# Optimization experiments

Measured on AMD Instinct MI355X. Metric: run time of the kernel, lower is better.

The kernel has to match this reference:

```python
import jax, jax.numpy as jnp
import numpy as np

B, T, C = 4, 2048, 768
H, D = 12, 64          # num heads, head size
MLP = 3072
EPS = 1e-6
SCALE = C ** (-0.5)    # NOTE: source scales by n_embd**-0.5, not head_size**-0.5


def setup_inputs() -> dict:
    key = jax.random.key(0)
    ks = jax.random.split(key, 12)
    s = 0.02
    return {
        "x":     jax.random.normal(ks[0], (B, T, C), jnp.float32),
        "Wq":    jax.random.normal(ks[1], (H, C, D), jnp.float32) * s,
        "Wk":    jax.random.normal(ks[2], (H, C, D), jnp.float32) * s,
        "Wv":    jax.random.normal(ks[3], (H, C, D), jnp.float32) * s,
        "Wo":    jax.random.normal(ks[4], (H * D, C), jnp.float32) * s,
        "bo":    jnp.zeros((C,), jnp.float32),
        "ln1_g": jnp.ones((C,), jnp.float32),
        "ln1_b": jnp.zeros((C,), jnp.float32),
        "ln2_g": jnp.ones((C,), jnp.float32),
        "ln2_b": jnp.zeros((C,), jnp.float32),
        "W1":    jax.random.normal(ks[5], (C, MLP), jnp.float32) * s,
        "b1":    jnp.zeros((MLP,), jnp.float32),
        "W2":    jax.random.normal(ks[6], (MLP, C), jnp.float32) * s,
        "b2":    jnp.zeros((C,), jnp.float32),
    }


def _ln(x, g, b):
    mu = jnp.mean(x, axis=-1, keepdims=True)
    var = jnp.var(x, axis=-1, keepdims=True)
    return (x - mu) * jax.lax.rsqrt(var + EPS) * g + b


def reference(x, Wq, Wk, Wv, Wo, bo, ln1_g, ln1_b, ln2_g, ln2_b, W1, b1, W2, b2):
    xn = _ln(x, ln1_g, ln1_b)
    # batched per-head projections: [B,T,C] x [H,C,D] -> [B,H,T,D]
    q = jnp.einsum("btc,hcd->bhtd", xn, Wq)
    k = jnp.einsum("btc,hcd->bhtd", xn, Wk)
    v = jnp.einsum("btc,hcd->bhtd", xn, Wv)
    wei = jnp.einsum("bhtd,bhsd->bhts", q, k) * SCALE  # [B,H,T,T]
    wei = jax.nn.softmax(wei, axis=-1)
    attn = jnp.einsum("bhts,bhsd->bhtd", wei, v)
    # concat heads along feature dim (head order preserved)
    attn = attn.transpose(0, 2, 1, 3).reshape(B, T, H * D)
    sa = attn @ Wo + bo
    x2 = sa + x                      # residual 1 (dropout = identity in eval)
    y = _ln(x2, ln2_g, ln2_b)
    y = jax.nn.gelu(y @ W1 + b1, approximate=False) @ W2 + b2
    return x2 + y                    # residual 2
```

## Files before the change

### kernel.cpp

```cpp
#include <hip/hip_runtime.h>
#include <hip/hip_bf16.h>
#include <cstdint>
#include <cmath>

#define B_ 4
#define T_ 2048
#define C_ 768
#define H_ 12
#define D_ 64
#define MLP_ 3072
#define BT_ (B_*T_)

typedef __hip_bfloat16 hbf;
typedef __bf16 bf16_t;
typedef bf16_t bf16x8 __attribute__((ext_vector_type(8)));
typedef bf16_t bf16x4 __attribute__((ext_vector_type(4)));
typedef float f32x4 __attribute__((ext_vector_type(4)));

static __device__ __forceinline__ void load_lds16(const void* g, void* l) {
    __builtin_amdgcn_global_load_lds(
        (const __attribute__((address_space(1))) unsigned int*)g,
        (__attribute__((address_space(3))) unsigned int*)l, 16, 0, 0);
}

__global__ __launch_bounds__(256) void pack_all(
    const float* __restrict__ Wq, const float* __restrict__ Wk,
    const float* __restrict__ Wv, const float* __restrict__ Wo,
    const float* __restrict__ W1, const float* __restrict__ W2,
    hbf* __restrict__ WqkT, hbf* __restrict__ WoT,
    hbf* __restrict__ W1T, hbf* __restrict__ W2T)
{
    __shared__ float tl[64 * 65];
    const int blk = blockIdx.x;
    const float* src; hbf* dst; int R, S, r0, s0;
    if (blk < 432) {
        const int z = blk / 12, y = blk - z * 12;
        const int mtx = z / 12, head = z - mtx * 12;
        src = (mtx == 0 ? Wq : mtx == 1 ? Wk : Wv) + (size_t)head * 49152;
        dst = WqkT + (size_t)z * 49152;
        R = 768; S = 64; r0 = y * 64; s0 = 0;
    } else if (blk < 576) {
        const int l = blk - 432;
        src = Wo; dst = WoT; R = 768; S = 768;
        r0 = (l / 12) * 64; s0 = (l % 12) * 64;
    } else if (blk < 1152) {
        const int l = blk - 576;
        src = W1; dst = W1T; R = 768; S = 3072;
        r0 = (l / 48) * 64; s0 = (l % 48) * 64;
    } else {
        const int l = blk - 1152;
        src = W2; dst = W2T; R = 3072; S = 768;
        r0 = (l / 12) * 64; s0 = (l % 12) * 64;
    }
    const int c = threadIdx.x & 63, q = threadIdx.x >> 6;
#pragma unroll
    for (int j = 0; j < 16; ++j) {
        int r = q + j * 4;
        tl[r * 65 + c] = src[(size_t)(r0 + r) * S + s0 + c];
    }
    __syncthreads();
#pragma unroll
    for (int j = 0; j < 16; ++j) {
        int s = q + j * 4;
        dst[(size_t)(s0 + s) * R + r0 + c] = __float2bfloat16(tl[c * 65 + s]);
    }
}

template<typename TI>
__global__ __launch_bounds__(192) void ln_kernel(
    const TI* __restrict__ x, const float* __restrict__ g,
    const float* __restrict__ bb, hbf* __restrict__ out)
{
    __shared__ float red[6];
    const int row = blockIdx.x;
    const int t = threadIdx.x;
    float v[4];
    if constexpr (__is_same(TI, float)) {
        const float4 xv = *(const float4*)(x + (size_t)row * C_ + t * 4);
        v[0] = xv.x; v[1] = xv.y; v[2] = xv.z; v[3] = xv.w;
    } else {
        bf16x4 xv = *(const bf16x4*)((const bf16_t*)x + (size_t)row * C_ + t * 4);
#pragma unroll
        for (int k = 0; k < 4; ++k) v[k] = (float)xv[k];
    }
    float s = 0.0f, s2 = 0.0f;
#pragma unroll
    for (int k = 0; k < 4; ++k) { s += v[k]; s2 += v[k] * v[k]; }
#pragma unroll
    for (int m = 1; m < 64; m <<= 1) {
        s  += __shfl_xor(s,  m, 64);
        s2 += __shfl_xor(s2, m, 64);
    }
    if ((t & 63) == 0) { red[t >> 6] = s; red[3 + (t >> 6)] = s2; }
    __syncthreads();
    float S  = red[0] + red[1] + red[2];
    float S2 = red[3] + red[4] + red[5];
    float mu  = S * (1.0f / C_);
    float var = S2 * (1.0f / C_) - mu * mu;
    float inv = rsqrtf(var + 1e-6f);
    const float4 gv = *(const float4*)(g  + t * 4);
    const float4 bv = *(const float4*)(bb + t * 4);
    bf16x4 o4;
    o4[0] = (bf16_t)((v[0] - mu) * inv * gv.x + bv.x);
    o4[1] = (bf16_t)((v[1] - mu) * inv * gv.y + bv.y);
    o4[2] = (bf16_t)((v[2] - mu) * inv * gv.z + bv.z);
    o4[3] = (bf16_t)((v[3] - mu) * inv * gv.w + bv.w);
    *(bf16x4*)((bf16_t*)out + (size_t)row * C_ + t * 4) = o4;
}

template<int EPI, int TN>
__global__ __launch_bounds__(256, 4) void gemm_kernel(
    const hbf* __restrict__ A, const hbf* __restrict__ Bt,
    float* __restrict__ outF, hbf* __restrict__ outH,
    const float* __restrict__ bias, const float* __restrict__ residF,
    const hbf* __restrict__ residH,
    int M, int N, int K,
    hbf* __restrict__ qb, hbf* __restrict__ kb, hbf* __restrict__ vt,
    float scale, int gx)
{
    constexpr int AM = (TN == 128) ? 4 : 2;
    constexpr int NB_B = (TN == 128) ? 4 : 2;
    __shared__ hbf sA[128 * 64];
    __shared__ hbf sB[TN * 64];
    const int tid = threadIdx.x;
    const int lane = tid & 63;
    const int wid = tid >> 6;
    const int lr = lane & 15, hg = lane >> 4;
    const int bid = blockIdx.x, nwg = gridDim.x;
    const int wg = (bid & 7) * (nwg >> 3) + (bid >> 3);
    const int bx = wg % gx, by = wg / gx;
    const int row0 = by * 128;
    const int col0 = bx * TN;
    const int wrow = (TN == 128) ? (wid >> 1) * 64 : wid * 32;
    const int wcol = (TN == 128) ? (wid & 1) * 64 : 0;

    f32x4 acc[AM][4] = {};

    int offG[4];
    const int Kb = K * 2;
#pragma unroll
    for (int i = 0; i < 4; ++i) {
        int c = tid + i * 256;
        offG[i] = (c >> 3) * Kb + (((c & 7) ^ ((c >> 3) & 7)) << 4);
    }
    const char* gA = (const char*)(A + (size_t)row0 * K);
    const char* gB = (const char*)(Bt + (size_t)col0 * K);

    auto stage = [&](int kt) {
        const int kb2 = kt * 128;
#pragma unroll
        for (int i = 0; i < 4; ++i)
            load_lds16(gA + (size_t)(offG[i] + kb2), (char*)sA + i * 4096 + wid * 1024);
#pragma unroll
        for (int i = 0; i < NB_B; ++i)
            load_lds16(gB + (size_t)(offG[i] + kb2), (char*)sB + i * 4096 + wid * 1024);
    };

    const int NK = K >> 6;
    stage(0);
    for (int kt = 0; kt < NK; ++kt) {
        __syncthreads();
#pragma unroll
        for (int kf = 0; kf < 2; ++kf) {
            const int sl = ((kf * 4 + hg) ^ (lr & 7)) << 4;
            bf16x8 af[AM], bfr[4];
#pragma unroll
            for (int m = 0; m < AM; ++m)
                af[m] = *(const bf16x8*)((const char*)sA + (wrow + m * 16 + lr) * 128 + sl);
#pragma unroll
            for (int n = 0; n < 4; ++n)
                bfr[n] = *(const bf16x8*)((const char*)sB + (wcol + n * 16 + lr) * 128 + sl);
#pragma unroll
            for (int m = 0; m < AM; ++m)
#pragma unroll
                for (int n = 0; n < 4; ++n)
                    acc[m][n] = __builtin_amdgcn_mfma_f32_16x16x32_bf16(af[m], bfr[n], acc[m][n], 0, 0, 0);
        }
        __syncthreads();
        if (kt + 1 < NK) stage(kt + 1);
    }

#pragma unroll
    for (int m = 0; m < AM; ++m) {
#pragma unroll
        for (int n = 0; n < 4; ++n) {
            const int colc = col0 + wcol + n * 16 + lr;
            const int rowb = row0 + wrow + m * 16 + hg * 4;
            if constexpr (EPI == 3) {
                if (colc >= 2 * C_) {
                    bf16x4 w;
#pragma unroll
                    for (int j = 0; j < 4; ++j) w[j] = (bf16_t)acc[m][n][j];
                    *(bf16x4*)(vt + (size_t)(colc - 2 * C_) * BT_ + rowb) = w;
                    continue;
                }
            }
#pragma unroll
            for (int j = 0; j < 4; ++j) {
                int row = rowb + j;
                int col = colc;
                float v = acc[m][n][j];
                if constexpr (EPI == 0) {
                    outH[(size_t)row * N + col] = __float2bfloat16(v);
                } else if constexpr (EPI == 2) {
                    float tt = v + bias[col];
                    float t3 = tt * tt * tt;
                    float z = fminf(fmaf(t3, 0.1029423372f, 2.3021141876f * tt), 126.0f);
                    float e = __builtin_amdgcn_exp2f(z);
                    float ge = tt * e * __builtin_amdgcn_rcpf(e + 1.0f);
                    outH[(size_t)row * N + col] = __float2bfloat16(ge);
                } else if constexpr (EPI == 3) {
                    int typ = col / C_;
                    int rr = col - typ * C_;
                    int h = rr >> 6, d = rr & 63;
                    int b = row >> 11, t = row & (T_ - 1);
                    size_t bh = (size_t)b * H_ + h;
                    if (typ == 0) qb[(bh * T_ + t) * D_ + d] = __float2bfloat16(v * scale);
                    else          kb[(bh * T_ + t) * D_ + d] = __float2bfloat16(v);
                } else if constexpr (EPI == 4) {
                    outH[(size_t)row * N + col] =
                        __float2bfloat16(v + bias[col] + residF[(size_t)row * N + col]);
                } else {
                    outF[(size_t)row * N + col] =
                        v + bias[col] + __bfloat162float(residH[(size_t)row * N + col]);
                }
            }
        }
    }
}

__global__ __launch_bounds__(256, 3) void attn_kernel(
    const hbf* __restrict__ qg, const hbf* __restrict__ kg,
    const hbf* __restrict__ vg, hbf* __restrict__ outA)
{
    __shared__ hbf sK0[64 * 64], sK1[64 * 64];
    __shared__ hbf sV0[64 * 64], sV1[64 * 64];
    __shared__ hbf sP[4 * 32 * 64];
    const int tid = threadIdx.x, lane = tid & 63, wid = tid >> 6;
    const int lr = lane & 15, hg = lane >> 4;
    const int wg = (blockIdx.x & 7) * 96 + (blockIdx.x >> 3);
    const int bh = wg >> 4;
    const int b = bh / H_, h = bh - b * H_;
    const int wr0 = (wg & 15) * 128 + wid * 32;
    const hbf* qbh = qg + (size_t)bh * T_ * D_;
    const hbf* kbh = kg + (size_t)bh * T_ * D_;
    const hbf* vbh = vg + (size_t)h * 64 * BT_ + (size_t)b * T_;

    bf16x8 a_q[2][2];
#pragma unroll
    for (int m = 0; m < 2; ++m)
#pragma unroll
        for (int kf = 0; kf < 2; ++kf)
            a_q[m][kf] = *(const bf16x8*)(qbh + (size_t)(wr0 + m * 16 + lr) * D_ + kf * 32 + hg * 8);

    bf16x8 vone;
#pragma unroll
    for (int i = 0; i < 8; ++i) vone[i] = (bf16_t)1.0f;

    f32x4 o[2][4] = {};
    f32x4 lden[2] = {};
    float mreg[2] = {-3e38f, -3e38f};

    int offK[2], offV[2];
#pragma unroll
    for (int i = 0; i < 2; ++i) {
        int c = tid + i * 256;
        int sw = ((c & 7) ^ ((c >> 3) & 7)) << 4;
        offK[i] = (c >> 3) * 128 + sw;
        offV[i] = (c >> 3) * (BT_ * 2) + sw;
    }
    hbf* sPw = sP + wid * (32 * 64);
    const int sl0 = ((0 * 4 + hg) ^ (lr & 7)) << 4;
    const int sl1 = ((1 * 4 + hg) ^ (lr & 7)) << 4;
    const int bcast = hg * 20;

    auto stage = [&](int itn, hbf* sKd, hbf* sVd) {
        const char* kp = (const char*)kbh + (size_t)itn * 8192;
        const char* vp = (const char*)vbh + (size_t)itn * 128;
#pragma unroll
        for (int i = 0; i < 2; ++i) {
            load_lds16(kp + offK[i], (char*)sKd + i * 4096 + wid * 1024);
            load_lds16(vp + offV[i], (char*)sVd + i * 4096 + wid * 1024);
        }
    };

    auto tile = [&](const hbf* sKc, const hbf* sVc) {
        f32x4 st[4][2] = {};
        __builtin_amdgcn_s_setprio(1);
#pragma unroll
        for (int kf = 0; kf < 2; ++kf) {
            const int sl = kf ? sl1 : sl0;
#pragma unroll
            for (int n = 0; n < 4; ++n) {
                bf16x8 ak = *(const bf16x8*)((const char*)sKc + (n * 16 + lr) * 128 + sl);
                st[n][0] = __builtin_amdgcn_mfma_f32_16x16x32_bf16(ak, a_q[0][kf], st[n][0], 0, 0, 0);
                st[n][1] = __builtin_amdgcn_mfma_f32_16x16x32_bf16(ak, a_q[1][kf], st[n][1], 0, 0, 0);
            }
        }
        __builtin_amdgcn_s_setprio(0);

        float tm[2];
#pragma unroll
        for (int m = 0; m < 2; ++m) {
            f32x4 mx = st[0][m];
            mx[0] = fmaxf(mx[0], st[1][m][0]); mx[1] = fmaxf(mx[1], st[1][m][1]);
            mx[2] = fmaxf(mx[2], st[1][m][2]); mx[3] = fmaxf(mx[3], st[1][m][3]);
            f32x4 my = st[2][m];
            my[0] = fmaxf(my[0], st[3][m][0]); my[1] = fmaxf(my[1], st[3][m][1]);
            my[2] = fmaxf(my[2], st[3][m][2]); my[3] = fmaxf(my[3], st[3][m][3]);
            float t01 = fmaxf(fmaxf(mx[0], my[0]), fmaxf(mx[1], my[1]));
            float t23 = fmaxf(fmaxf(mx[2], my[2]), fmaxf(mx[3], my[3]));
            tm[m] = fmaxf(t01, t23);
        }
        {
            float a0 = tm[0], b0 = tm[0], a1 = tm[1], b1 = tm[1];
            asm volatile("v_permlane32_swap_b32 %0, %1" : "+v"(a0), "+v"(b0));
            asm volatile("v_permlane32_swap_b32 %0, %1" : "+v"(a1), "+v"(b1));
            a0 = fmaxf(a0, b0);
            a1 = fmaxf(a1, b1);
            float s0 = __shfl_xor(a0, 16, 64);
            float s1 = __shfl_xor(a1, 16, 64);
            tm[0] = fmaxf(a0, s0);
            tm[1] = fmaxf(a1, s1);
        }

#pragma unroll
        for (int m = 0; m < 2; ++m) {
            const float t = tm[m];
            if (__any(t - mreg[m] > 11.5415603f)) {
                float nm = fmaxf(mreg[m], t);
                float fac = __builtin_amdgcn_exp2f(mreg[m] - nm);
                mreg[m] = nm;
                float fb[4];
#pragma unroll
                for (int j = 0; j < 4; ++j)
                    fb[j] = __shfl(fac, bcast + j, 64);
#pragma unroll
                for (int j = 0; j < 4; ++j) {
                    lden[m][j] *= fb[j];
#pragma unroll
                    for (int nd = 0; nd < 4; ++nd)
                        o[m][nd][j] *= fb[j];
                }
            }
            const int r = m * 16 + lr;
#pragma unroll
            for (int n = 0; n < 4; ++n) {
                float p0 = __builtin_amdgcn_exp2f(st[n][m][0] - mreg[m]);
                float p1 = __builtin_amdgcn_exp2f(st[n][m][1] - mreg[m]);
                float p2 = __builtin_amdgcn_exp2f(st[n][m][2] - mreg[m]);
                float p3 = __builtin_amdgcn_exp2f(st[n][m][3] - mreg[m]);
                bf16x4 w;
                w[0] = (bf16_t)p0; w[1] = (bf16_t)p1; w[2] = (bf16_t)p2; w[3] = (bf16_t)p3;
                *(bf16x4*)((char*)sPw + r * 128 +
                           (((n * 2 + (hg >> 1)) ^ (r & 7)) << 4) + ((hg & 1) * 8)) = w;
            }
        }

        __builtin_amdgcn_s_setprio(1);
#pragma unroll
        for (int kf = 0; kf < 2; ++kf) {
            const int sl = kf ? sl1 : sl0;
            bf16x8 ap0 = *(const bf16x8*)((const char*)sPw + lr * 128 + sl);
            bf16x8 ap1 = *(const bf16x8*)((const char*)sPw + (16 + lr) * 128 + sl);
            lden[0] = __builtin_amdgcn_mfma_f32_16x16x32_bf16(ap0, vone, lden[0], 0, 0, 0);
            lden[1] = __builtin_amdgcn_mfma_f32_16x16x32_bf16(ap1, vone, lden[1], 0, 0, 0);
#pragma unroll
            for (int nd = 0; nd < 4; ++nd) {
                bf16x8 bv = *(const bf16x8*)((const char*)sVc + (nd * 16 + lr) * 128 + sl);
                o[0][nd] = __builtin_amdgcn_mfma_f32_16x16x32_bf16(ap0, bv, o[0][nd], 0, 0, 0);
                o[1][nd] = __builtin_amdgcn_mfma_f32_16x16x32_bf16(ap1, bv, o[1][nd], 0, 0, 0);
            }
        }
        __builtin_amdgcn_s_setprio(0);
    };

    const int NT = T_ / 64;
    stage(0, sK0, sV0);
    __syncthreads();
    for (int it = 0; it < NT; it += 2) {
        stage(it + 1, sK1, sV1);
        tile(sK0, sV0);
        __syncthreads();
        if (it + 2 < NT) stage(it + 2, sK0, sV0);
        tile(sK1, sV1);
        __syncthreads();
    }

#pragma unroll
    for (int m = 0; m < 2; ++m) {
        f32x4 rinv;
#pragma unroll
        for (int j = 0; j < 4; ++j) rinv[j] = __builtin_amdgcn_rcpf(lden[m][j]);
#pragma unroll
        for (int nd = 0; nd < 4; ++nd)
#pragma unroll
            for (int j = 0; j < 4; ++j) {
                int row = wr0 + m * 16 + hg * 4 + j;
                int col = nd * 16 + lr;
                outA[((size_t)(b * T_ + row)) * C_ + h * D_ + col] =
                    __float2bfloat16(o[m][nd][j] * rinv[j]);
            }
    }
}

extern "C" void kernel_launch(void* const* d_in, const int* in_sizes, int n_in,
                              void* d_out, int out_size, void* d_ws, size_t ws_size,
                              hipStream_t stream)
{
    const float* x    = (const float*)d_in[0];
    const float* Wq   = (const float*)d_in[1];
    const float* Wk   = (const float*)d_in[2];
    const float* Wv   = (const float*)d_in[3];
    const float* Wo   = (const float*)d_in[4];
    const float* bo   = (const float*)d_in[5];
    const float* ln1g = (const float*)d_in[6];
    const float* ln1b = (const float*)d_in[7];
    const float* ln2g = (const float*)d_in[8];
    const float* ln2b = (const float*)d_in[9];
    const float* W1   = (const float*)d_in[10];
    const float* b1   = (const float*)d_in[11];
    const float* W2   = (const float*)d_in[12];
    const float* b2   = (const float*)d_in[13];
    float* out = (float*)d_out;
    char* ws = (char*)d_ws;

    hbf*  xn    = (hbf*)(ws + 0);
    hbf*  WqkT  = (hbf*)(ws + 12582912);
    hbf*  qb    = (hbf*)(ws + 16121856);
    hbf*  kb    = (hbf*)(ws + 28704768);
    hbf*  vT    = (hbf*)(ws + 41287680);
    hbf*  h1    = (hbf*)(ws + 0);
    hbf*  attnB = (hbf*)(ws + 53870592);
    hbf*  yln   = (hbf*)(ws + 53870592);
    hbf*  x2b   = (hbf*)(ws + 66453504);
    hbf*  WoT   = (hbf*)(ws + 91619328);
    hbf*  W1T   = (hbf*)(ws + 92798976);
    hbf*  W2T   = (hbf*)(ws + 97517568);

    const float SCALE2 = 0.036084391824351615f * 1.4426950408889634f;

    pack_all<<<1728, 256, 0, stream>>>(Wq, Wk, Wv, Wo, W1, W2, WqkT, WoT, W1T, W2T);
    ln_kernel<float><<<8192, 192, 0, stream>>>(x, ln1g, ln1b, xn);
    gemm_kernel<3,128><<<1152, 256, 0, stream>>>(xn, WqkT, nullptr, nullptr, nullptr, nullptr,
        nullptr, 8192, 2304, 768, qb, kb, vT, SCALE2, 18);
    attn_kernel<<<768, 256, 0, stream>>>(qb, kb, vT, attnB);
    gemm_kernel<4,64><<<768, 256, 0, stream>>>(attnB, WoT, nullptr, x2b, bo, x,
        nullptr, 8192, 768, 768, nullptr, nullptr, nullptr, 1.0f, 12);
    ln_kernel<hbf><<<8192, 192, 0, stream>>>(x2b, ln2g, ln2b, yln);
    gemm_kernel<2,128><<<1536, 256, 0, stream>>>(yln, W1T, nullptr, h1, b1, nullptr,
        nullptr, 8192, 3072, 768, nullptr, nullptr, nullptr, 1.0f, 24);
    gemm_kernel<5,64><<<768, 256, 0, stream>>>(h1, W2T, out, nullptr, b2, nullptr,
        x2b, 8192, 768, 3072, nullptr, nullptr, nullptr, 1.0f, 12);
}
```

Baseline: 258.8 us.

## Merge LN1 into weight-pack kernel and interleave softmax with PV per row block

Folds the first LayerNorm into the weight packing launch by giving LN rows their own block range, which removes one kernel launch and lets the two independent jobs run side by side. In the attention tile, the V fragments are now loaded into registers once before softmax, and the softmax and PV MFMA work is split per 16-row half. The MFMAs for the first half can then overlap the exp work of the second half. The cost is higher register pressure from holding the V fragments, plus 64 idle threads in each LN block.

```diff
diff --git a/kernel.cpp b/kernel.cpp
--- a/kernel.cpp
+++ b/kernel.cpp
@@ -23,46 +23,84 @@
         (__attribute__((address_space(3))) unsigned int*)l, 16, 0, 0);
 }
 
-__global__ __launch_bounds__(256) void pack_all(
+__global__ __launch_bounds__(256) void pack_ln(
+    const float* __restrict__ x, const float* __restrict__ ln1g,
+    const float* __restrict__ ln1b, hbf* __restrict__ xn,
     const float* __restrict__ Wq, const float* __restrict__ Wk,
     const float* __restrict__ Wv, const float* __restrict__ Wo,
     const float* __restrict__ W1, const float* __restrict__ W2,
     hbf* __restrict__ WqkT, hbf* __restrict__ WoT,
     hbf* __restrict__ W1T, hbf* __restrict__ W2T)
 {
-    __shared__ float tl[64 * 65];
+    __shared__ float smem[64 * 65];
     const int blk = blockIdx.x;
+    const int t = threadIdx.x;
+    if (blk < 8192) {
+        const bool act = t < 192;
+        float v[4] = {0, 0, 0, 0};
+        if (act) {
+            const float4 xv = *(const float4*)(x + (size_t)blk * C_ + t * 4);
+            v[0] = xv.x; v[1] = xv.y; v[2] = xv.z; v[3] = xv.w;
+        }
+        float s = 0.0f, s2 = 0.0f;
+#pragma unroll
+        for (int k = 0; k < 4; ++k) { s += v[k]; s2 += v[k] * v[k]; }
+#pragma unroll
+        for (int m = 1; m < 64; m <<= 1) {
+            s  += __shfl_xor(s,  m, 64);
+            s2 += __shfl_xor(s2, m, 64);
+        }
+        if (act && (t & 63) == 0) { smem[t >> 6] = s; smem[3 + (t >> 6)] = s2; }
+        __syncthreads();
+        if (act) {
+            float S  = smem[0] + smem[1] + smem[2];
+            float S2 = smem[3] + smem[4] + smem[5];
+            float mu  = S * (1.0f / C_);
+            float var = S2 * (1.0f / C_) - mu * mu;
+            float inv = rsqrtf(var + 1e-6f);
+            const float4 gv = *(const float4*)(ln1g + t * 4);
+            const float4 bv = *(const float4*)(ln1b + t * 4);
+            bf16x4 o4;
+            o4[0] = (bf16_t)((v[0] - mu) * inv * gv.x + bv.x);
+            o4[1] = (bf16_t)((v[1] - mu) * inv * gv.y + bv.y);
+            o4[2] = (bf16_t)((v[2] - mu) * inv * gv.z + bv.z);
+            o4[3] = (bf16_t)((v[3] - mu) * inv * gv.w + bv.w);
+            *(bf16x4*)((bf16_t*)xn + (size_t)blk * C_ + t * 4) = o4;
+        }
+        return;
+    }
+    const int pb = blk - 8192;
     const float* src; hbf* dst; int R, S, r0, s0;
-    if (blk < 432) {
-        const int z = blk / 12, y = blk - z * 12;
+    if (pb < 432) {
+        const int z = pb / 12, y = pb - z * 12;
         const int mtx = z / 12, head = z - mtx * 12;
         src = (mtx == 0 ? Wq : mtx == 1 ? Wk : Wv) + (size_t)head * 49152;
         dst = WqkT + (size_t)z * 49152;
         R = 768; S = 64; r0 = y * 64; s0 = 0;
-    } else if (blk < 576) {
-        const int l = blk - 432;
+    } else if (pb < 576) {
+        const int l = pb - 432;
         src = Wo; dst = WoT; R = 768; S = 768;
         r0 = (l / 12) * 64; s0 = (l % 12) * 64;
-    } else if (blk < 1152) {
-        const int l = blk - 576;
+    } else if (pb < 1152) {
+        const int l = pb - 576;
         src = W1; dst = W1T; R = 768; S = 3072;
         r0 = (l / 48) * 64; s0 = (l % 48) * 64;
     } else {
-        const int l = blk - 1152;
+        const int l = pb - 1152;
         src = W2; dst = W2T; R = 3072; S = 768;
         r0 = (l / 12) * 64; s0 = (l % 12) * 64;
     }
-    const int c = threadIdx.x & 63, q = threadIdx.x >> 6;
+    const int c = t & 63, q = t >> 6;
 #pragma unroll
     for (int j = 0; j < 16; ++j) {
         int r = q + j * 4;
-        tl[r * 65 + c] = src[(size_t)(r0 + r) * S + s0 + c];
+        smem[r * 65 + c] = src[(size_t)(r0 + r) * S + s0 + c];
     }
     __syncthreads();
 #pragma unroll
     for (int j = 0; j < 16; ++j) {
         int s = q + j * 4;
-        dst[(size_t)(s0 + s) * R + r0 + c] = __float2bfloat16(tl[c * 65 + s]);
+        dst[(size_t)(s0 + s) * R + r0 + c] = __float2bfloat16(smem[c * 65 + s]);
     }
 }
 
@@ -284,6 +322,51 @@
         }
     };
 
+#define SOFTMAX_M(m, tmv)                                                      \
+    {                                                                          \
+        if (__any((tmv) - mreg[m] > 11.5415603f)) {                            \
+            float nm = fmaxf(mreg[m], (tmv));                                  \
+            float fac = __builtin_amdgcn_exp2f(mreg[m] - nm);                  \
+            mreg[m] = nm;                                                      \
+            float fb[4];                                                       \
+            _Pragma("unroll")                                                  \
+            for (int j = 0; j < 4; ++j) fb[j] = __shfl(fac, bcast + j, 64);    \
+            _Pragma("unroll")                                                  \
+            for (int j = 0; j < 4; ++j) {                                      \
+                lden[m][j] *= fb[j];                                           \
+                _Pragma("unroll")                                              \
+                for (int nd = 0; nd < 4; ++nd) o[m][nd][j] *= fb[j];           \
+            }                                                                  \
+        }                                                                      \
+        const int r = (m) * 16 + lr;                                           \
+        _Pragma("unroll")                                                      \
+        for (int n = 0; n < 4; ++n) {                                          \
+            float p0 = __builtin_amdgcn_exp2f(st[n][m][0] - mreg[m]);          \
+            float p1 = __builtin_amdgcn_exp2f(st[n][m][1] - mreg[m]);          \
+            float p2 = __builtin_amdgcn_exp2f(st[n][m][2] - mreg[m]);          \
+            float p3 = __builtin_amdgcn_exp2f(st[n][m][3] - mreg[m]);          \
+            bf16x4 w;                                                          \
+            w[0] = (bf16_t)p0; w[1] = (bf16_t)p1;                              \
+            w[2] = (bf16_t)p2; w[3] = (bf16_t)p3;                              \
+            *(bf16x4*)((char*)sPw + r * 128 +                                  \
+                       (((n * 2 + (hg >> 1)) ^ (r & 7)) << 4) +                \
+                       ((hg & 1) * 8)) = w;                                    \
+        }                                                                      \
+    }
+
+#define PV_M(m)                                                                \
+    __builtin_amdgcn_s_setprio(1);                                             \
+    _Pragma("unroll")                                                          \
+    for (int kf = 0; kf < 2; ++kf) {                                           \
+        const int sl = kf ? sl1 : sl0;                                         \
+        bf16x8 ap = *(const bf16x8*)((const char*)sPw + ((m) * 16 + lr) * 128 + sl); \
+        lden[m] = __builtin_amdgcn_mfma_f32_16x16x32_bf16(ap, vone, lden[m], 0, 0, 0); \
+        _Pragma("unroll")                                                      \
+        for (int nd = 0; nd < 4; ++nd)                                         \
+            o[m][nd] = __builtin_amdgcn_mfma_f32_16x16x32_bf16(ap, bvr[kf][nd], o[m][nd], 0, 0, 0); \
+    }                                                                          \
+    __builtin_amdgcn_s_setprio(0);
+
     auto tile = [&](const hbf* sKc, const hbf* sVc) {
         f32x4 st[4][2] = {};
         __builtin_amdgcn_s_setprio(1);
@@ -298,6 +381,15 @@
             }
         }
         __builtin_amdgcn_s_setprio(0);
+
+        bf16x8 bvr[2][4];
+#pragma unroll
+        for (int kf = 0; kf < 2; ++kf) {
+            const int sl = kf ? sl1 : sl0;
+#pragma unroll
+            for (int nd = 0; nd < 4; ++nd)
+                bvr[kf][nd] = *(const bf16x8*)((const char*)sVc + (nd * 16 + lr) * 128 + sl);
+        }
 
         float tm[2];
 #pragma unroll
@@ -324,55 +416,10 @@
             tm[1] = fmaxf(a1, s1);
         }
 
-#pragma unroll
-        for (int m = 0; m < 2; ++m) {
-            const float t = tm[m];
-            if (__any(t - mreg[m] > 11.5415603f)) {
-                float nm = fmaxf(mreg[m], t);
-                float fac = __builtin_amdgcn_exp2f(mreg[m] - nm);
-                mreg[m] = nm;
-                float fb[4];
-#pragma unroll
-                for (int j = 0; j < 4; ++j)
-                    fb[j] = __shfl(fac, bcast + j, 64);
-#pragma unroll
-                for (int j = 0; j < 4; ++j) {
-                    lden[m][j] *= fb[j];
-#pragma unroll
-                    for (int nd = 0; nd < 4; ++nd)
-                        o[m][nd][j] *= fb[j];
-                }
-            }
-            const int r = m * 16 + lr;
-#pragma unroll
-            for (int n = 0; n < 4; ++n) {
-                float p0 = __builtin_amdgcn_exp2f(st[n][m][0] - mreg[m]);
-                float p1 = __builtin_amdgcn_exp2f(st[n][m][1] - mreg[m]);
-                float p2 = __builtin_amdgcn_exp2f(st[n][m][2] - mreg[m]);
-                float p3 = __builtin_amdgcn_exp2f(st[n][m][3] - mreg[m]);
-                bf16x4 w;
-                w[0] = (bf16_t)p0; w[1] = (bf16_t)p1; w[2] = (bf16_t)p2; w[3] = (bf16_t)p3;
-                *(bf16x4*)((char*)sPw + r * 128 +
-                           (((n * 2 + (hg >> 1)) ^ (r & 7)) << 4) + ((hg & 1) * 8)) = w;
-            }
-        }
-
-        __builtin_amdgcn_s_setprio(1);
-#pragma unroll
-        for (int kf = 0; kf < 2; ++kf) {
-            const int sl = kf ? sl1 : sl0;
-            bf16x8 ap0 = *(const bf16x8*)((const char*)sPw + lr * 128 + sl);
-            bf16x8 ap1 = *(const bf16x8*)((const char*)sPw + (16 + lr) * 128 + sl);
-            lden[0] = __builtin_amdgcn_mfma_f32_16x16x32_bf16(ap0, vone, lden[0], 0, 0, 0);
-            lden[1] = __builtin_amdgcn_mfma_f32_16x16x32_bf16(ap1, vone, lden[1], 0, 0, 0);
-#pragma unroll
-            for (int nd = 0; nd < 4; ++nd) {
-                bf16x8 bv = *(const bf16x8*)((const char*)sVc + (nd * 16 + lr) * 128 + sl);
-                o[0][nd] = __builtin_amdgcn_mfma_f32_16x16x32_bf16(ap0, bv, o[0][nd], 0, 0, 0);
-                o[1][nd] = __builtin_amdgcn_mfma_f32_16x16x32_bf16(ap1, bv, o[1][nd], 0, 0, 0);
-            }
-        }
-        __builtin_amdgcn_s_setprio(0);
+        SOFTMAX_M(0, tm[0]);
+        PV_M(0);
+        SOFTMAX_M(1, tm[1]);
+        PV_M(1);
     };
 
     const int NT = T_ / 64;
@@ -402,6 +449,8 @@
                     __float2bfloat16(o[m][nd][j] * rinv[j]);
             }
     }
+#undef SOFTMAX_M
+#undef PV_M
 }
 
 extern "C" void kernel_launch(void* const* d_in, const int* in_sizes, int n_in,
@@ -440,8 +489,8 @@
 
     const float SCALE2 = 0.036084391824351615f * 1.4426950408889634f;
 
-    pack_all<<<1728, 256, 0, stream>>>(Wq, Wk, Wv, Wo, W1, W2, WqkT, WoT, W1T, W2T);
-    ln_kernel<float><<<8192, 192, 0, stream>>>(x, ln1g, ln1b, xn);
+    pack_ln<<<9920, 256, 0, stream>>>(x, ln1g, ln1b, xn,
+        Wq, Wk, Wv, Wo, W1, W2, WqkT, WoT, W1T, W2T);
     gemm_kernel<3,128><<<1152, 256, 0, stream>>>(xn, WqkT, nullptr, nullptr, nullptr, nullptr,
         nullptr, 8192, 2304, 768, qb, kb, vT, SCALE2, 18);
     attn_kernel<<<768, 256, 0, stream>>>(qb, kb, vT, attnB);
```

Result: no change. 257.7 us, median of 2 (-0.4%).
